# Kernel optimization log

Hardware: AMD Instinct MI355X
Metric: run time of the kernel (lower is better)

Reference implementation:

```python
import jax, jax.numpy as jnp
import numpy as np

D = 64          # cfg.D_PAIR
NT = 6          # cfg.N_TORSION_OUT
LN_EPS = 1e-5


def _layernorm(x, g, b):
    # torch LayerNorm computed in float32 then cast back
    x32 = x.astype(jnp.float32)
    m = jnp.mean(x32, axis=-1, keepdims=True)
    v = jnp.var(x32, axis=-1, keepdims=True)
    y = (x32 - m) / jnp.sqrt(v + LN_EPS) * g + b
    return y.astype(x.dtype)


def setup_inputs() -> dict:
    key = jax.random.key(0)
    ks = jax.random.split(key, 16)
    B, L = 2, 512
    s = 0.125  # ~xavier scale for fan 64
    inp = {
        "pair": jax.random.normal(ks[0], (B, L, L, D), jnp.float32),
        "torsion": jax.random.normal(ks[1], (B, L, NT), jnp.float32),
        "ln_g": jnp.ones((D,), jnp.float32),
        "ln_b": jnp.zeros((D,), jnp.float32),
        "Wl": jax.random.normal(ks[2], (D, D), jnp.float32) * s,
        "Wr": jax.random.normal(ks[3], (D, D), jnp.float32) * s,
        "Wlg": jax.random.normal(ks[4], (D, D), jnp.float32) * s,
        "blg": jnp.zeros((D,), jnp.float32),
        "Wrg": jax.random.normal(ks[5], (D, D), jnp.float32) * s,
        "brg": jnp.zeros((D,), jnp.float32),
        "Wog": jax.random.normal(ks[6], (D, D), jnp.float32) * s,
        "bog": jnp.zeros((D,), jnp.float32),
        "Wout": jax.random.normal(ks[7], (D, D), jnp.float32) * s,  # 'final' init is zeros; randomized to exercise math
        "bout": jnp.zeros((D,), jnp.float32),
        "lno_g": jnp.ones((D,), jnp.float32),
        "lno_b": jnp.zeros((D,), jnp.float32),
        "Wt": jax.random.normal(ks[8], (1, NT), jnp.float32) * 0.4,
        "bt": jnp.zeros((1,), jnp.float32),
    }
    return inp


def reference(pair, torsion, ln_g, ln_b, Wl, Wr, Wlg, blg, Wrg, brg,
              Wog, bog, Wout, bout, lno_g, lno_b, Wt, bt):
    B, L, _, d = pair.shape
    z = _layernorm(pair, ln_g, ln_b)                         # [B,L,L,D]
    a = (z @ Wl.T) * jax.nn.sigmoid(z @ Wlg.T + blg)         # left proj * gate
    b = (z @ Wr.T) * jax.nn.sigmoid(z @ Wrg.T + brg)         # right proj * gate
    t_w = jax.nn.sigmoid(torsion @ Wt.T + bt)[..., 0]        # [B,L]
    # outgoing=True branch: tw unsqueezed to [B,1,L,1] then transposed(1,2) -> [B,L,1,1]
    a_w = a * t_w[:, :, None, None]
    x = jnp.einsum('bikd,bjkd->bijd', a_w, b) / (L ** 0.5 + 1e-8)
    g = jax.nn.sigmoid(z @ Wog.T + bog)
    out = (_layernorm(x, lno_g, lno_b) @ Wout.T + bout) * g
    return pair + out
```

## Files before the change

kernel.cpp:

```cpp
#include <hip/hip_runtime.h>
#include <stdint.h>

#define LL 512
#define DD 64

typedef __attribute__((ext_vector_type(8))) short bf16x8;
typedef __attribute__((ext_vector_type(4))) float f32x4;

#define MFMA16(a, b, c) __builtin_amdgcn_mfma_f32_16x16x32_bf16((a), (b), (c), 0, 0, 0)

__device__ __forceinline__ float bf2f(unsigned short u) {
    union { unsigned int i; float f; } v; v.i = ((unsigned int)u) << 16; return v.f;
}
__device__ __forceinline__ unsigned short f2bf(float f) {
    union { float f; unsigned int i; } v; v.f = f;
    unsigned int i = v.i;
    return (unsigned short)((i + 0x7FFFu + ((i >> 16) & 1u)) >> 16);
}
__device__ __forceinline__ float sigm(float x) {
    float d = 1.0f + __expf(-x);
    float y = __builtin_amdgcn_rcpf(d);
    return y * __builtin_fmaf(-d, y, 2.0f);
}

__global__ void prep_w(const float* __restrict__ Wl, const float* __restrict__ Wr,
                       const float* __restrict__ Wlg, const float* __restrict__ Wrg,
                       const float* __restrict__ Wog, const float* __restrict__ Wout,
                       unsigned short* __restrict__ Wcat, unsigned short* __restrict__ WoutB) {
    int t = threadIdx.x + blockIdx.x * blockDim.x;
    int stride = blockDim.x * gridDim.x;
    for (int idx = t; idx < 320 * 64; idx += stride) {
        int row = idx >> 6, col = idx & 63;
        int sec = row >> 6, r = row & 63;
        float v;
        switch (sec) {
            case 0:  v = Wl[r * 64 + col];  break;
            case 1:  v = Wlg[r * 64 + col]; break;
            case 2:  v = Wr[r * 64 + col];  break;
            case 3:  v = Wrg[r * 64 + col]; break;
            default: v = Wog[r * 64 + col]; break;
        }
        Wcat[idx] = f2bf(v);
    }
    for (int idx = t; idx < 64 * 64; idx += stride) WoutB[idx] = f2bf(Wout[idx]);
}

__launch_bounds__(256)
__global__ void k1_proj(const float* __restrict__ pair, const float* __restrict__ torsion,
                        const float* __restrict__ ln_g, const float* __restrict__ ln_b,
                        const float* __restrict__ blg, const float* __restrict__ brg,
                        const float* __restrict__ bog, const float* __restrict__ Wt,
                        const float* __restrict__ bt, const unsigned short* __restrict__ Wcat,
                        unsigned short* __restrict__ At2, unsigned short* __restrict__ Bt2,
                        unsigned short* __restrict__ G) {
    const int cj = blockIdx.x;
    const int a  = blockIdx.y;
    const int bb = blockIdx.z;
    const int c0j = cj * 32;
    const int t = threadIdx.x, w = t >> 6, lane = t & 63;
    const int rsel = lane & 15, koff = lane >> 4;
    const int col = w * 16 + rsel;
    __shared__ unsigned short zs[128][72];
    __shared__ unsigned short awL[64][136];
    __shared__ unsigned short bL[64][136];

    float tw4[4];
    #pragma unroll
    for (int il = 0; il < 4; ++il) {
        float acc = bt[0];
        #pragma unroll
        for (int n = 0; n < 6; ++n)
            acc += torsion[((size_t)(bb * LL + 4 * a + il)) * 6 + n] * Wt[n];
        tw4[il] = sigm(acc);
    }

    bf16x8 wfr[5][2];
    #pragma unroll
    for (int s = 0; s < 5; ++s)
        #pragma unroll
        for (int kh = 0; kh < 2; ++kh)
            wfr[s][kh] = *(const bf16x8*)&Wcat[(size_t)(s * 64 + col) * 64 + kh * 32 + koff * 8];
    const float vblg = blg[col], vbrg = brg[col], vbog = bog[col];

    {
        const int sub = lane & 3, rr = lane >> 2;
        const float4* pr4 = (const float4*)(pair +
            (((size_t)(bb * LL + 4 * a + w) * LL) + c0j) * DD);
        #pragma unroll
        for (int p = 0; p < 2; ++p) {
            const int rl = p * 16 + rr;
            float4 x[4];
            #pragma unroll
            for (int q = 0; q < 4; ++q) x[q] = pr4[rl * 16 + sub * 4 + q];
            float s = 0.f, s2 = 0.f;
            #pragma unroll
            for (int q = 0; q < 4; ++q) {
                s += x[q].x + x[q].y + x[q].z + x[q].w;
                s2 += x[q].x * x[q].x + x[q].y * x[q].y + x[q].z * x[q].z + x[q].w * x[q].w;
            }
            s += __shfl_xor(s, 1);  s2 += __shfl_xor(s2, 1);
            s += __shfl_xor(s, 2);  s2 += __shfl_xor(s2, 2);
            float m = s * 0.015625f;
            float var = s2 * 0.015625f - m * m;
            float rstd = rsqrtf(var + 1e-5f);
            #pragma unroll
            for (int q = 0; q < 4; ++q) {
                float4 lg4 = ((const float4*)ln_g)[sub * 4 + q];
                float4 lb4 = ((const float4*)ln_b)[sub * 4 + q];
                ushort4 zw;
                zw.x = f2bf((x[q].x - m) * rstd * lg4.x + lb4.x);
                zw.y = f2bf((x[q].y - m) * rstd * lg4.y + lb4.y);
                zw.z = f2bf((x[q].z - m) * rstd * lg4.z + lb4.z);
                zw.w = f2bf((x[q].w - m) * rstd * lg4.w + lb4.w);
                *(ushort4*)&zs[w * 32 + rl][sub * 16 + q * 4] = zw;
            }
        }
    }
    __syncthreads();

    ushort4 gk[8];
    #pragma unroll
    for (int mi = 0; mi < 8; ++mi) {
        bf16x8 a0 = *(const bf16x8*)&zs[mi * 16 + rsel][koff * 8];
        bf16x8 a1 = *(const bf16x8*)&zs[mi * 16 + rsel][32 + koff * 8];
        f32x4 pl = {0.f, 0.f, 0.f, 0.f}, plg = pl, pr = pl, prg = pl, pog = pl;
        pl  = MFMA16(a0, wfr[0][0], pl);  pl  = MFMA16(a1, wfr[0][1], pl);
        plg = MFMA16(a0, wfr[1][0], plg); plg = MFMA16(a1, wfr[1][1], plg);
        pr  = MFMA16(a0, wfr[2][0], pr);  pr  = MFMA16(a1, wfr[2][1], pr);
        prg = MFMA16(a0, wfr[3][0], prg); prg = MFMA16(a1, wfr[3][1], prg);
        pog = MFMA16(a0, wfr[4][0], pog); pog = MFMA16(a1, wfr[4][1], pog);

        const float tww = tw4[mi >> 1];
        const int crow = mi * 16 + koff * 4;
        unsigned short aw4[4], bm4[4], g4[4];
        #pragma unroll
        for (int r = 0; r < 4; ++r) {
            float av = pl[r] * sigm(plg[r] + vblg) * tww;
            float bv = pr[r] * sigm(prg[r] + vbrg);
            float gv = sigm(pog[r] + vbog);
            aw4[r] = f2bf(av); bm4[r] = f2bf(bv); g4[r] = f2bf(gv);
        }
        *(ushort4*)&awL[col][crow] = make_ushort4(aw4[0], aw4[1], aw4[2], aw4[3]);
        *(ushort4*)&bL[col][crow]  = make_ushort4(bm4[0], bm4[1], bm4[2], bm4[3]);
        gk[mi] = make_ushort4(g4[0], g4[1], g4[2], g4[3]);
    }
    __syncthreads();

    #pragma unroll
    for (int mi = 0; mi < 8; ++mi) {
        const int rbase = mi * 16 + koff * 4;
        zs[rbase + 0][col] = gk[mi].x;
        zs[rbase + 1][col] = gk[mi].y;
        zs[rbase + 2][col] = gk[mi].z;
        zs[rbase + 3][col] = gk[mi].w;
    }
    __syncthreads();

    const int itb = a >> 5;
    const int wmb = (a >> 4) & 1;
    const int mif = (a >> 2) & 3;
    const int ri0 = (a & 3) * 4;
    {
        const int il = t & 3, g = (t >> 2) & 3, dlow = t >> 4;
        const int lfrag = g * 16 + ri0 + il;
        #pragma unroll
        for (int q = 0; q < 4; ++q) {
            const int d = q * 16 + dlow;
            const int p = bb * 64 + d;
            size_t base = (((size_t)(p * 4 + itb) * 16 + cj) * 4096)
                        + wmb * 2048 + mif * 512 + (size_t)lfrag * 8;
            *(uint4*)&At2[base] = *(const uint4*)&awL[d][il * 32 + g * 8];
            *(uint4*)&Bt2[base] = *(const uint4*)&bL[d][il * 32 + g * 8];
        }
    }
    #pragma unroll
    for (int it8 = 0; it8 < 8; ++it8) {
        int r = it8 * 16 + (t >> 4), cc = (t & 15) * 4;
        size_t pos = ((size_t)(bb * LL + 4 * a + (r >> 5)) * LL) + c0j + (r & 31);
        *(ushort4*)&G[pos * DD + cc] = *(const ushort4*)&zs[r][cc];
    }
}

__launch_bounds__(256, 4)
__global__ void k2_gemm(const unsigned short* __restrict__ At2,
                        const unsigned short* __restrict__ Bt2,
                        unsigned short* __restrict__ Xt) {
    int lin = blockIdx.x + (blockIdx.y << 4);
    int nlin = (lin & 7) * 256 + (lin >> 3);
    const int p = nlin >> 4;
    const int tile = nlin & 15;
    const int it = tile >> 2, jt = tile & 3;
    const int i0 = it * 128, j0 = jt * 128;
    const int t = threadIdx.x, lane = t & 63, w = t >> 6;
    const int wm = w >> 1, wn = w & 1;
    __shared__ unsigned short Cs[128][136];

    f32x4 acc[4][4];
    #pragma unroll
    for (int i = 0; i < 4; ++i)
        #pragma unroll
        for (int j = 0; j < 4; ++j) acc[i][j] = (f32x4){0.f, 0.f, 0.f, 0.f};

    const unsigned short* ap = At2 + ((size_t)(p * 4 + it) * 16) * 4096
                             + wm * 2048 + lane * 8;
    const unsigned short* bp = Bt2 + ((size_t)(p * 4 + jt) * 16) * 4096
                             + wn * 2048 + lane * 8;

    #pragma unroll 4
    for (int k = 0; k < 16; ++k) {
        bf16x8 af[4], bfr[4];
        #pragma unroll
        for (int mi = 0; mi < 4; ++mi)
            af[mi] = *(const bf16x8*)(ap + (size_t)k * 4096 + mi * 512);
        #pragma unroll
        for (int ni = 0; ni < 4; ++ni)
            bfr[ni] = *(const bf16x8*)(bp + (size_t)k * 4096 + ni * 512);
        #pragma unroll
        for (int mi = 0; mi < 4; ++mi)
            #pragma unroll
            for (int ni = 0; ni < 4; ++ni)
                acc[mi][ni] = MFMA16(af[mi], bfr[ni], acc[mi][ni]);
    }

    const int rsel = lane & 15, koff = lane >> 4;
    const float s = 1.0f / (sqrtf((float)LL) + 1e-8f);
    #pragma unroll
    for (int mi = 0; mi < 4; ++mi)
        #pragma unroll
        for (int ni = 0; ni < 4; ++ni)
            #pragma unroll
            for (int r = 0; r < 4; ++r)
                Cs[wm * 64 + mi * 16 + koff * 4 + r][wn * 64 + ni * 16 + rsel] =
                    f2bf(acc[mi][ni][r] * s);
    __syncthreads();
    #pragma unroll
    for (int it8 = 0; it8 < 8; ++it8) {
        int row = it8 * 16 + (t >> 4), colc = (t & 15) * 8;
        uint4 v = *(const uint4*)&Cs[row][colc];
        *(uint4*)&Xt[((size_t)p * LL + i0 + row) * LL + j0 + colc] = v;
    }
}

__launch_bounds__(256)
__global__ void k3_out(const unsigned short* __restrict__ Xt, const unsigned short* __restrict__ G,
                       const float* __restrict__ pairIn, const unsigned short* __restrict__ WoutB,
                       const float* __restrict__ lno_g, const float* __restrict__ lno_b,
                       const float* __restrict__ bout, float* __restrict__ out) {
    const int bb = blockIdx.z, irow = blockIdx.y, c0 = blockIdx.x * 128;
    const int t = threadIdx.x, w = t >> 6, lane = t & 63;
    __shared__ unsigned short x1[64][128];
    __shared__ unsigned short x2[128][72];

    #pragma unroll
    for (int q = 0; q < 4; ++q) {
        int idx = t + q * 256, d = idx >> 4, c8 = idx & 15;
        uint4 v = *(const uint4*)&Xt[((size_t)(bb * 64 + d) * LL + irow) * LL + c0 + c8 * 8];
        *(uint4*)&x1[d][c8 * 8] = v;
    }
    __syncthreads();
    {
        const int c = t & 127, half = t >> 7;
        unsigned short tmp[32];
        #pragma unroll
        for (int dd = 0; dd < 32; ++dd) tmp[dd] = x1[half * 32 + dd][c];
        #pragma unroll
        for (int q = 0; q < 4; ++q)
            *(uint4*)&x2[c][half * 32 + q * 8] = *(const uint4*)&tmp[q * 8];
    }
    __syncthreads();

    {
        const int sub = lane & 3, rr = lane >> 2;
        #pragma unroll
        for (int p = 0; p < 2; ++p) {
            const int row = w * 32 + p * 16 + rr;
            ushort4 raw[4];
            #pragma unroll
            for (int q = 0; q < 4; ++q) raw[q] = *(const ushort4*)&x2[row][sub * 16 + q * 4];
            float xv[16];
            #pragma unroll
            for (int q = 0; q < 4; ++q) {
                xv[q * 4 + 0] = bf2f(raw[q].x);
                xv[q * 4 + 1] = bf2f(raw[q].y);
                xv[q * 4 + 2] = bf2f(raw[q].z);
                xv[q * 4 + 3] = bf2f(raw[q].w);
            }
            float s = 0.f, s2 = 0.f;
            #pragma unroll
            for (int e = 0; e < 16; ++e) { s += xv[e]; s2 += xv[e] * xv[e]; }
            s += __shfl_xor(s, 1);  s2 += __shfl_xor(s2, 1);
            s += __shfl_xor(s, 2);  s2 += __shfl_xor(s2, 2);
            float m = s * 0.015625f;
            float var = s2 * 0.015625f - m * m;
            float rstd = rsqrtf(var + 1e-5f);
            #pragma unroll
            for (int q = 0; q < 4; ++q) {
                float4 lg4 = ((const float4*)lno_g)[sub * 4 + q];
                float4 lb4 = ((const float4*)lno_b)[sub * 4 + q];
                ushort4 zw;
                zw.x = f2bf((xv[q * 4 + 0] - m) * rstd * lg4.x + lb4.x);
                zw.y = f2bf((xv[q * 4 + 1] - m) * rstd * lg4.y + lb4.y);
                zw.z = f2bf((xv[q * 4 + 2] - m) * rstd * lg4.z + lb4.z);
                zw.w = f2bf((xv[q * 4 + 3] - m) * rstd * lg4.w + lb4.w);
                *(ushort4*)&x2[row][sub * 16 + q * 4] = zw;
            }
        }
    }
    __syncthreads();

    unsigned short* o_lds = &x1[0][0];
    const int rsel = lane & 15, koff = lane >> 4;
    #pragma unroll
    for (int mh = 0; mh < 2; ++mh) {
        const int mi = 2 * w + mh;
        bf16x8 a0 = *(const bf16x8*)&x2[mi * 16 + rsel][koff * 8];
        bf16x8 a1 = *(const bf16x8*)&x2[mi * 16 + rsel][32 + koff * 8];
        #pragma unroll
        for (int n = 0; n < 4; ++n) {
            f32x4 pacc = {0.f, 0.f, 0.f, 0.f};
            const unsigned short* wrow = WoutB + (size_t)(n * 16 + rsel) * 64;
            pacc = MFMA16(a0, *(const bf16x8*)&wrow[koff * 8], pacc);
            pacc = MFMA16(a1, *(const bf16x8*)&wrow[32 + koff * 8], pacc);
            const float bo = bout[n * 16 + rsel];
            #pragma unroll
            for (int r = 0; r < 4; ++r)
                o_lds[(mi * 16 + koff * 4 + r) * 64 + n * 16 + rsel] = f2bf(pacc[r] + bo);
        }
    }
    __syncthreads();

    #pragma unroll
    for (int q = 0; q < 4; ++q) {
        int e = q * 2048 + t * 8;
        int c = e >> 6, o = e & 63;
        size_t pos = (size_t)(bb * LL + irow) * LL + c0 + c;
        uint4 ov = *(const uint4*)&o_lds[c * 64 + o];
        uint4 gv = *(const uint4*)&G[pos * DD + o];
        const unsigned short* ovp = (const unsigned short*)&ov;
        const unsigned short* gvp = (const unsigned short*)&gv;
        float4 p0 = *(const float4*)&pairIn[pos * DD + o];
        float4 p1 = *(const float4*)&pairIn[pos * DD + o + 4];
        float4 r0, r1;
        r0.x = p0.x + bf2f(ovp[0]) * bf2f(gvp[0]);
        r0.y = p0.y + bf2f(ovp[1]) * bf2f(gvp[1]);
        r0.z = p0.z + bf2f(ovp[2]) * bf2f(gvp[2]);
        r0.w = p0.w + bf2f(ovp[3]) * bf2f(gvp[3]);
        r1.x = p1.x + bf2f(ovp[4]) * bf2f(gvp[4]);
        r1.y = p1.y + bf2f(ovp[5]) * bf2f(gvp[5]);
        r1.z = p1.z + bf2f(ovp[6]) * bf2f(gvp[6]);
        r1.w = p1.w + bf2f(ovp[7]) * bf2f(gvp[7]);
        *(float4*)&out[pos * DD + o] = r0;
        *(float4*)&out[pos * DD + o + 4] = r1;
    }
}

extern "C" void kernel_launch(void* const* d_in, const int* in_sizes, int n_in,
                              void* d_out, int out_size, void* d_ws, size_t ws_size,
                              hipStream_t stream) {
    const float* pair    = (const float*)d_in[0];
    const float* torsion = (const float*)d_in[1];
    const float* ln_g    = (const float*)d_in[2];
    const float* ln_b    = (const float*)d_in[3];
    const float* Wl      = (const float*)d_in[4];
    const float* Wr      = (const float*)d_in[5];
    const float* Wlg     = (const float*)d_in[6];
    const float* blg     = (const float*)d_in[7];
    const float* Wrg     = (const float*)d_in[8];
    const float* brg     = (const float*)d_in[9];
    const float* Wog     = (const float*)d_in[10];
    const float* bog     = (const float*)d_in[11];
    const float* Wout    = (const float*)d_in[12];
    const float* bout    = (const float*)d_in[13];
    const float* lno_g   = (const float*)d_in[14];
    const float* lno_b   = (const float*)d_in[15];
    const float* Wt      = (const float*)d_in[16];
    const float* bt      = (const float*)d_in[17];
    float* outp = (float*)d_out;

    const size_t PLANE_B = (size_t)128 * LL * LL * 2;
    const size_t need = 4 * PLANE_B + (320 * 64 + 64 * 64) * 2;
    if (ws_size < need) return;

    char* ws = (char*)d_ws;
    unsigned short* At2   = (unsigned short*)(ws);
    unsigned short* Bt2   = (unsigned short*)(ws + PLANE_B);
    unsigned short* G     = (unsigned short*)(ws + 2 * PLANE_B);
    unsigned short* Xt    = (unsigned short*)(ws + 3 * PLANE_B);
    unsigned short* Wcat  = (unsigned short*)(ws + 4 * PLANE_B);
    unsigned short* WoutB = Wcat + 320 * 64;

    prep_w<<<dim3(40), dim3(256), 0, stream>>>(Wl, Wr, Wlg, Wrg, Wog, Wout, Wcat, WoutB);
    k1_proj<<<dim3(16, 128, 2), dim3(256), 0, stream>>>(pair, torsion, ln_g, ln_b, blg, brg,
                                                        bog, Wt, bt, Wcat, At2, Bt2, G);
    k2_gemm<<<dim3(16, 128), dim3(256), 0, stream>>>(At2, Bt2, Xt);
    k3_out<<<dim3(4, LL, 2), dim3(256), 0, stream>>>(Xt, G, pair, WoutB, lno_g, lno_b, bout, outp);
}
```

Before: 260.5 us.

## Double-buffer GEMM fragment loads and repad projection LDS tiles

The batched GEMM kernel now software-pipelines its global fragment loads with two register buffers, so the next k-step's A/B fragments are in flight while MFMAs run on the current ones. Occupancy hint drops from 4 to 3 blocks to make room for the extra registers. In the projection kernel the LDS row padding changes from 136 to 132 and reads are split into two 8-byte loads, aiming to reduce bank conflicts in the transpose-out. The cost is lower occupancy and narrower LDS reads.

```diff
diff --git a/kernel.cpp b/kernel.cpp
--- a/kernel.cpp
+++ b/kernel.cpp
@@ -61,8 +61,8 @@
     const int rsel = lane & 15, koff = lane >> 4;
     const int col = w * 16 + rsel;
     __shared__ unsigned short zs[128][72];
-    __shared__ unsigned short awL[64][136];
-    __shared__ unsigned short bL[64][136];
+    __shared__ unsigned short awL[64][132];
+    __shared__ unsigned short bL[64][132];
 
     float tw4[4];
     #pragma unroll
@@ -169,8 +169,12 @@
             const int p = bb * 64 + d;
             size_t base = (((size_t)(p * 4 + itb) * 16 + cj) * 4096)
                         + wmb * 2048 + mif * 512 + (size_t)lfrag * 8;
-            *(uint4*)&At2[base] = *(const uint4*)&awL[d][il * 32 + g * 8];
-            *(uint4*)&Bt2[base] = *(const uint4*)&bL[d][il * 32 + g * 8];
+            uint2 alo = *(const uint2*)&awL[d][il * 32 + g * 8];
+            uint2 ahi = *(const uint2*)&awL[d][il * 32 + g * 8 + 4];
+            uint2 blo = *(const uint2*)&bL[d][il * 32 + g * 8];
+            uint2 bhi = *(const uint2*)&bL[d][il * 32 + g * 8 + 4];
+            *(uint4*)&At2[base] = make_uint4(alo.x, alo.y, ahi.x, ahi.y);
+            *(uint4*)&Bt2[base] = make_uint4(blo.x, blo.y, bhi.x, bhi.y);
         }
     }
     #pragma unroll
@@ -181,7 +185,7 @@
     }
 }
 
-__launch_bounds__(256, 4)
+__launch_bounds__(256, 3)
 __global__ void k2_gemm(const unsigned short* __restrict__ At2,
                         const unsigned short* __restrict__ Bt2,
                         unsigned short* __restrict__ Xt) {
@@ -206,20 +210,36 @@
     const unsigned short* bp = Bt2 + ((size_t)(p * 4 + jt) * 16) * 4096
                              + wn * 2048 + lane * 8;
 
-    #pragma unroll 4
-    for (int k = 0; k < 16; ++k) {
-        bf16x8 af[4], bfr[4];
+    bf16x8 aA[4], bA[4], aB[4], bB[4];
+    #pragma unroll
+    for (int m = 0; m < 4; ++m) {
+        aA[m] = *(const bf16x8*)(ap + m * 512);
+        bA[m] = *(const bf16x8*)(bp + m * 512);
+    }
+    #pragma unroll
+    for (int kk = 0; kk < 8; ++kk) {
+        #pragma unroll
+        for (int m = 0; m < 4; ++m) {
+            aB[m] = *(const bf16x8*)(ap + (size_t)(2 * kk + 1) * 4096 + m * 512);
+            bB[m] = *(const bf16x8*)(bp + (size_t)(2 * kk + 1) * 4096 + m * 512);
+        }
         #pragma unroll
         for (int mi = 0; mi < 4; ++mi)
-            af[mi] = *(const bf16x8*)(ap + (size_t)k * 4096 + mi * 512);
-        #pragma unroll
-        for (int ni = 0; ni < 4; ++ni)
-            bfr[ni] = *(const bf16x8*)(bp + (size_t)k * 4096 + ni * 512);
+            #pragma unroll
+            for (int ni = 0; ni < 4; ++ni)
+                acc[mi][ni] = MFMA16(aA[mi], bA[ni], acc[mi][ni]);
+        if (kk < 7) {
+            #pragma unroll
+            for (int m = 0; m < 4; ++m) {
+                aA[m] = *(const bf16x8*)(ap + (size_t)(2 * kk + 2) * 4096 + m * 512);
+                bA[m] = *(const bf16x8*)(bp + (size_t)(2 * kk + 2) * 4096 + m * 512);
+            }
+        }
         #pragma unroll
         for (int mi = 0; mi < 4; ++mi)
             #pragma unroll
             for (int ni = 0; ni < 4; ++ni)
-                acc[mi][ni] = MFMA16(af[mi], bfr[ni], acc[mi][ni]);
+                acc[mi][ni] = MFMA16(aB[mi], bB[ni], acc[mi][ni]);
     }
 
     const int rsel = lane & 15, koff = lane >> 4;
```

After: 254.2 us. -2.4%, faster.
